# Kernel tuning notes

Hardware: AMD Instinct MI355X
Metric: run time of the kernel (lower is better)

Reference implementation:

```python
import jax, jax.numpy as jnp
import numpy as np

N_NODES = 50000
N_EDGES = 800000
IN, HID, OUT = 96, 96, 64


def setup_inputs() -> dict:
    key = jax.random.key(0)
    ks = jax.random.split(key, 12)
    x = jax.random.normal(ks[0], (N_NODES, IN), dtype=jnp.float32)
    src = jax.random.randint(ks[1], (N_EDGES,), 0, N_NODES, dtype=jnp.int32)
    dst = jax.random.randint(ks[2], (N_EDGES,), 0, N_NODES, dtype=jnp.int32)
    dims = [(IN, HID), (HID, HID), (HID, OUT)]
    params = {}
    for i, (din, dout) in enumerate(dims):
        s = 1.0 / np.sqrt(din)
        params[f"w_self{i}"] = jax.random.uniform(ks[3 + 3 * i], (dout, din), jnp.float32, -s, s)
        params[f"w_neigh{i}"] = jax.random.uniform(ks[4 + 3 * i], (dout, din), jnp.float32, -s, s)
        params[f"b{i}"] = jnp.zeros((dout,), jnp.float32)
    return {"x": x, "src": src, "dst": dst, **params}


def _sage_layer(h, src, dst, w_self, w_neigh, b):
    # mean aggregation of source-node features onto destination nodes
    msum = jax.ops.segment_sum(h[src], dst, num_segments=N_NODES)  # [N, d]
    deg = jax.ops.segment_sum(jnp.ones((src.shape[0],), h.dtype), dst, num_segments=N_NODES)
    hmean = msum / jnp.maximum(deg, 1.0)[:, None]
    return h @ w_self.T + hmean @ w_neigh.T + b


def reference(x, src, dst,
              w_self0, w_neigh0, b0,
              w_self1, w_neigh1, b1,
              w_self2, w_neigh2, b2):
    # Layer 0 + ReLU (dropout is identity in eval mode)
    h = jax.nn.relu(_sage_layer(x, src, dst, w_self0, w_neigh0, b0))
    # Layer 1 + ReLU
    h = jax.nn.relu(_sage_layer(h, src, dst, w_self1, w_neigh1, b1))
    # Final layer, no activation
    h = _sage_layer(h, src, dst, w_self2, w_neigh2, b2)
    return h
```

## Files before the change

kernel.cpp:

```cpp
#include <hip/hip_runtime.h>
#include <hip/hip_fp16.h>


#define DIN 96

typedef __attribute__((ext_vector_type(8))) short bf16x8;
typedef __attribute__((ext_vector_type(16))) float f32x16;

__global__ void zero_deg_kernel(int* __restrict__ p, int n) {
    int i = blockIdx.x * blockDim.x + threadIdx.x;
    if (i < n) p[i] = 0;
}

__global__ void deg_kernel(const int* __restrict__ dst, int* __restrict__ deg,
                           int* __restrict__ rank, int nE) {
    int i = blockIdx.x * blockDim.x + threadIdx.x;
    if (i < nE) rank[i] = atomicAdd(&deg[dst[i]], 1);
}

__global__ void block_sum_kernel(const int* __restrict__ deg, int* __restrict__ bsum, int nN) {
    __shared__ int s[256];
    const int tid = threadIdx.x;
    int i = blockIdx.x * 256 + tid;
    s[tid] = (i < nN) ? deg[i] : 0;
    __syncthreads();
    for (int d = 128; d > 0; d >>= 1) {
        if (tid < d) s[tid] += s[tid + d];
        __syncthreads();
    }
    if (tid == 0) bsum[blockIdx.x] = s[0];
}

__global__ void bsum_scan_kernel(int* __restrict__ bsum, int nB) {
    __shared__ int s[256];
    const int tid = threadIdx.x;
    int v = (tid < nB) ? bsum[tid] : 0;
    s[tid] = v;
    __syncthreads();
    for (int d = 1; d < 256; d <<= 1) {
        int t = (tid >= d) ? s[tid - d] : 0;
        __syncthreads();
        s[tid] += t;
        __syncthreads();
    }
    if (tid < nB) bsum[tid] = s[tid] - v;
}

__global__ void scan_apply_kernel(const int* __restrict__ deg, const int* __restrict__ bsum,
                                  int* __restrict__ offs, int nN) {
    __shared__ int s[256];
    const int tid = threadIdx.x;
    int i = blockIdx.x * 256 + tid;
    int v = (i < nN) ? deg[i] : 0;
    s[tid] = v;
    __syncthreads();
    for (int d = 1; d < 256; d <<= 1) {
        int t = (tid >= d) ? s[tid - d] : 0;
        __syncthreads();
        s[tid] += t;
        __syncthreads();
    }
    if (i < nN) offs[i] = bsum[blockIdx.x] + s[tid] - v;
}

__global__ void bucket_kernel(const int* __restrict__ src, const int* __restrict__ dst,
                              const int* __restrict__ offs, const int* __restrict__ rank,
                              unsigned short* __restrict__ esrc, int nE) {
    int e = blockIdx.x * blockDim.x + threadIdx.x;
    if (e < nE) esrc[offs[dst[e]] + rank[e]] = (unsigned short)src[e];
}

__global__ void tof16_kernel(const float* __restrict__ x, __half* __restrict__ xf, int n8) {
    int i = blockIdx.x * blockDim.x + threadIdx.x;
    if (i >= n8) return;
    float4 f0 = *reinterpret_cast<const float4*>(x + (size_t)i * 8);
    float4 f1 = *reinterpret_cast<const float4*>(x + (size_t)i * 8 + 4);
    union { __half2 h2[4]; float4 raw; } o;
    o.h2[0] = __float22half2_rn(make_float2(f0.x, f0.y));
    o.h2[1] = __float22half2_rn(make_float2(f0.z, f0.w));
    o.h2[2] = __float22half2_rn(make_float2(f1.x, f1.y));
    o.h2[3] = __float22half2_rn(make_float2(f1.z, f1.w));
    *reinterpret_cast<float4*>(xf + (size_t)i * 8) = o.raw;
}

__global__ void gather_kernel(const __half* __restrict__ hf, const unsigned short* __restrict__ esrc,
                              const int* __restrict__ offs, const int* __restrict__ deg,
                              __half* __restrict__ hmean, int nN) {
    int idx = blockIdx.x * blockDim.x + threadIdx.x;
    if (idx >= nN * 12) return;
    int n = idx / 12;
    int q = idx - n * 12;
    const int beg = offs[n];
    const int dg = deg[n];
    const int end = beg + dg;
    const __half* hq = hf + q * 8;

    union H8 { float4 raw; __half2 h2[4]; };
    float a0[8], a1[8], a2[8], a3[8];
#pragma unroll
    for (int k = 0; k < 8; ++k) { a0[k] = 0.f; a1[k] = 0.f; a2[k] = 0.f; a3[k] = 0.f; }

    int j = beg;
    for (; j + 4 <= end; j += 4) {
        int s0 = esrc[j], s1 = esrc[j + 1], s2 = esrc[j + 2], s3 = esrc[j + 3];
        H8 v0, v1, v2, v3;
        v0.raw = *reinterpret_cast<const float4*>(hq + (size_t)s0 * DIN);
        v1.raw = *reinterpret_cast<const float4*>(hq + (size_t)s1 * DIN);
        v2.raw = *reinterpret_cast<const float4*>(hq + (size_t)s2 * DIN);
        v3.raw = *reinterpret_cast<const float4*>(hq + (size_t)s3 * DIN);
#pragma unroll
        for (int k = 0; k < 4; ++k) {
            float2 f0 = __half22float2(v0.h2[k]);
            float2 f1 = __half22float2(v1.h2[k]);
            float2 f2 = __half22float2(v2.h2[k]);
            float2 f3 = __half22float2(v3.h2[k]);
            a0[2 * k] += f0.x; a0[2 * k + 1] += f0.y;
            a1[2 * k] += f1.x; a1[2 * k + 1] += f1.y;
            a2[2 * k] += f2.x; a2[2 * k + 1] += f2.y;
            a3[2 * k] += f3.x; a3[2 * k + 1] += f3.y;
        }
    }
    for (; j < end; ++j) {
        int s0 = esrc[j];
        H8 v0;
        v0.raw = *reinterpret_cast<const float4*>(hq + (size_t)s0 * DIN);
#pragma unroll
        for (int k = 0; k < 4; ++k) {
            float2 f0 = __half22float2(v0.h2[k]);
            a0[2 * k] += f0.x; a0[2 * k + 1] += f0.y;
        }
    }
    const float r = 1.0f / (float)max(dg, 1);
    union H8 o;
    o.h2[0] = __float22half2_rn(make_float2((a0[0]+a1[0]+a2[0]+a3[0])*r, (a0[1]+a1[1]+a2[1]+a3[1])*r));
    o.h2[1] = __float22half2_rn(make_float2((a0[2]+a1[2]+a2[2]+a3[2])*r, (a0[3]+a1[3]+a2[3]+a3[3])*r));
    o.h2[2] = __float22half2_rn(make_float2((a0[4]+a1[4]+a2[4]+a3[4])*r, (a0[5]+a1[5]+a2[5]+a3[5])*r));
    o.h2[3] = __float22half2_rn(make_float2((a0[6]+a1[6]+a2[6]+a3[6])*r, (a0[7]+a1[7]+a2[7]+a3[7])*r));
    *reinterpret_cast<float4*>(hmean + (size_t)n * DIN + q * 8) = o.raw;
}

__device__ __forceinline__ void fv8_to_hilo(const float* fv, bf16x8& hi, bf16x8& lo) {
    union { unsigned int u[4]; bf16x8 v; } H, L;
#pragma unroll
    for (int i = 0; i < 4; ++i) {
        unsigned u0 = __float_as_uint(fv[2 * i]);
        unsigned u1 = __float_as_uint(fv[2 * i + 1]);
        unsigned h0 = u0 & 0xFFFF0000u;
        unsigned h1 = u1 & 0xFFFF0000u;
        H.u[i] = h1 | (h0 >> 16);
        float l0 = fv[2 * i]     - __uint_as_float(h0);
        float l1 = fv[2 * i + 1] - __uint_as_float(h1);
        L.u[i] = (__float_as_uint(l1) & 0xFFFF0000u) | (__float_as_uint(l0) >> 16);
    }
    hi = H.v; lo = L.v;
}

template<int DOUT, int NP, bool RELU, bool WF16>
__global__ __launch_bounds__(256)
void sage_gemm_mfma(const float* __restrict__ hin, const __half* __restrict__ hm16,
                    const float* __restrict__ wself, const float* __restrict__ wneigh,
                    const float* __restrict__ bias, float* __restrict__ hout,
                    __half* __restrict__ fout, int nN) {
    __shared__ unsigned int WhiS[DOUT][100];
    __shared__ unsigned int WloS[DOUT][100];

    const int tid = threadIdx.x;
    const int n0 = blockIdx.x * 256;

    for (int c = tid; c < DOUT * 24; c += 256) {
        int r = c / 24, k8 = c - (c / 24) * 24;
        const float* srcw = (k8 < 12) ? (wself + (size_t)r * 96 + k8 * 8)
                                      : (wneigh + (size_t)r * 96 + (k8 - 12) * 8);
        float4 f0 = *reinterpret_cast<const float4*>(srcw);
        float4 f1 = *reinterpret_cast<const float4*>(srcw + 4);
        float fv[8] = {f0.x, f0.y, f0.z, f0.w, f1.x, f1.y, f1.z, f1.w};
        bf16x8 hi, lo;
        fv8_to_hilo(fv, hi, lo);
        *reinterpret_cast<bf16x8*>(&WhiS[r][k8 * 4]) = hi;
        *reinterpret_cast<bf16x8*>(&WloS[r][k8 * 4]) = lo;
    }
    __syncthreads();

    const int lane = tid & 63;
    const int w = tid >> 6;
    const int col = lane & 31;
    const int q = lane >> 5;
    const int mbase = n0 + w * 64;

    const int nA0 = min(mbase + col, nN - 1);
    const int nA1 = min(mbase + 32 + col, nN - 1);

    f32x16 acc[NP][2];
#pragma unroll
    for (int p = 0; p < NP; ++p) {
        f32x16 z = {};
        acc[p][0] = z;
        acc[p][1] = z;
    }

#pragma unroll
    for (int ks = 0; ks < 12; ++ks) {
        float fv0[8], fv1[8];
        if (ks < 6) {
            const float* s0 = hin + (size_t)nA0 * 96 + ks * 16 + q * 8;
            const float* s1 = hin + (size_t)nA1 * 96 + ks * 16 + q * 8;
            float4 a = *reinterpret_cast<const float4*>(s0);
            float4 b = *reinterpret_cast<const float4*>(s0 + 4);
            float4 c = *reinterpret_cast<const float4*>(s1);
            float4 d = *reinterpret_cast<const float4*>(s1 + 4);
            fv0[0]=a.x; fv0[1]=a.y; fv0[2]=a.z; fv0[3]=a.w;
            fv0[4]=b.x; fv0[5]=b.y; fv0[6]=b.z; fv0[7]=b.w;
            fv1[0]=c.x; fv1[1]=c.y; fv1[2]=c.z; fv1[3]=c.w;
            fv1[4]=d.x; fv1[5]=d.y; fv1[6]=d.z; fv1[7]=d.w;
        } else {
            const __half* s0 = hm16 + (size_t)nA0 * 96 + (ks - 6) * 16 + q * 8;
            const __half* s1 = hm16 + (size_t)nA1 * 96 + (ks - 6) * 16 + q * 8;
            union { float4 raw; __half2 h2[4]; } u0, u1;
            u0.raw = *reinterpret_cast<const float4*>(s0);
            u1.raw = *reinterpret_cast<const float4*>(s1);
#pragma unroll
            for (int k = 0; k < 4; ++k) {
                float2 f0 = __half22float2(u0.h2[k]);
                float2 f1 = __half22float2(u1.h2[k]);
                fv0[2 * k] = f0.x; fv0[2 * k + 1] = f0.y;
                fv1[2 * k] = f1.x; fv1[2 * k + 1] = f1.y;
            }
        }
        bf16x8 ahi0, alo0, ahi1, alo1;
        fv8_to_hilo(fv0, ahi0, alo0);
        fv8_to_hilo(fv1, ahi1, alo1);

#pragma unroll
        for (int p = 0; p < NP; ++p) {
            const bf16x8 whi = *reinterpret_cast<const bf16x8*>(&WhiS[p * 32 + col][ks * 8 + q * 4]);
            const bf16x8 wlo = *reinterpret_cast<const bf16x8*>(&WloS[p * 32 + col][ks * 8 + q * 4]);
            acc[p][0] = __builtin_amdgcn_mfma_f32_32x32x16_bf16(ahi0, whi, acc[p][0], 0, 0, 0);
            acc[p][0] = __builtin_amdgcn_mfma_f32_32x32x16_bf16(ahi0, wlo, acc[p][0], 0, 0, 0);
            acc[p][0] = __builtin_amdgcn_mfma_f32_32x32x16_bf16(alo0, whi, acc[p][0], 0, 0, 0);
            acc[p][1] = __builtin_amdgcn_mfma_f32_32x32x16_bf16(ahi1, whi, acc[p][1], 0, 0, 0);
            acc[p][1] = __builtin_amdgcn_mfma_f32_32x32x16_bf16(ahi1, wlo, acc[p][1], 0, 0, 0);
            acc[p][1] = __builtin_amdgcn_mfma_f32_32x32x16_bf16(alo1, whi, acc[p][1], 0, 0, 0);
        }
    }

#pragma unroll
    for (int p = 0; p < NP; ++p) {
        const int oc = p * 32 + col;
        const float bv = bias[oc];
#pragma unroll
        for (int i = 0; i < 16; ++i) {
            const int row = (i & 3) + 8 * (i >> 2) + 4 * q;
            int n = mbase + row;
            if (n < nN) {
                float v = acc[p][0][i] + bv;
                if (RELU) v = fmaxf(v, 0.f);
                hout[(size_t)n * DOUT + oc] = v;
                if (WF16) fout[(size_t)n * DOUT + oc] = __float2half_rn(v);
            }
            n = mbase + 32 + row;
            if (n < nN) {
                float v = acc[p][1][i] + bv;
                if (RELU) v = fmaxf(v, 0.f);
                hout[(size_t)n * DOUT + oc] = v;
                if (WF16) fout[(size_t)n * DOUT + oc] = __float2half_rn(v);
            }
        }
    }
}

extern "C" void kernel_launch(void* const* d_in, const int* in_sizes, int n_in,
                              void* d_out, int out_size, void* d_ws, size_t ws_size,
                              hipStream_t stream) {
    const float* x   = (const float*)d_in[0];
    const int*   src = (const int*)d_in[1];
    const int*   dst = (const int*)d_in[2];
    const float* ws0 = (const float*)d_in[3];
    const float* wn0 = (const float*)d_in[4];
    const float* b0  = (const float*)d_in[5];
    const float* ws1 = (const float*)d_in[6];
    const float* wn1 = (const float*)d_in[7];
    const float* b1  = (const float*)d_in[8];
    const float* ws2 = (const float*)d_in[9];
    const float* wn2 = (const float*)d_in[10];
    const float* b2  = (const float*)d_in[11];
    float* out = (float*)d_out;

    const int nN = in_sizes[0] / DIN;
    const int nE = in_sizes[1];
    const int nB = (nN + 255) / 256;

    int* deg  = (int*)d_ws;
    int* offs = deg + 50048;
    int* bsum = offs + 50048;
    int* rank = bsum + 256;
    unsigned short* esrc = (unsigned short*)(rank + nE);
    __half* hm16 = (__half*)(esrc + nE);
    float* hA    = (float*)(hm16 + (size_t)nN * DIN);
    float* hB    = hA + (size_t)nN * DIN;

    __half* f16buf = (__half*)d_out;

    zero_deg_kernel<<<nB, 256, 0, stream>>>(deg, nN);
    deg_kernel<<<(nE + 255) / 256, 256, 0, stream>>>(dst, deg, rank, nE);
    block_sum_kernel<<<nB, 256, 0, stream>>>(deg, bsum, nN);
    bsum_scan_kernel<<<1, 256, 0, stream>>>(bsum, nB);
    scan_apply_kernel<<<nB, 256, 0, stream>>>(deg, bsum, offs, nN);
    bucket_kernel<<<(nE + 255) / 256, 256, 0, stream>>>(src, dst, offs, rank, esrc, nE);

    const int ggrid = (nN * 12 + 255) / 256;
    const int mgrid = (nN + 255) / 256;

    tof16_kernel<<<ggrid, 256, 0, stream>>>(x, f16buf, nN * 12);
    gather_kernel<<<ggrid, 256, 0, stream>>>(f16buf, esrc, offs, deg, hm16, nN);
    sage_gemm_mfma<96, 3, true, true><<<mgrid, 256, 0, stream>>>(x, hm16, ws0, wn0, b0, hA, f16buf, nN);

    gather_kernel<<<ggrid, 256, 0, stream>>>(f16buf, esrc, offs, deg, hm16, nN);
    sage_gemm_mfma<96, 3, true, true><<<mgrid, 256, 0, stream>>>(hA, hm16, ws1, wn1, b1, hB, f16buf, nN);

    gather_kernel<<<ggrid, 256, 0, stream>>>(f16buf, esrc, offs, deg, hm16, nN);
    sage_gemm_mfma<64, 2, false, false><<<mgrid, 256, 0, stream>>>(hB, hm16, ws2, wn2, b2, out, nullptr, nN);
}
```

Before: 222.8 us.

## Use wave-per-node edge-parallel gather and fp16-only hidden activations in GEMMs

The gather kernel now assigns one 64-lane wave per node: 60 lanes cover 5 edges times 12 feature chunks at a time, and a cross-lane shuffle reduction sums the partial results. This is meant to balance uneven degrees and give more loads in flight per node. The GEMM now reads self features as fp16 and writes only the fp16 hidden output in place, dropping the fp32 hidden buffers and their reads and writes. The trade-off is lower precision on the self-feature path, including the input x, plus 4 idle lanes per wave and shuffle overhead.

```diff
diff --git a/kernel.cpp b/kernel.cpp
--- a/kernel.cpp
+++ b/kernel.cpp
@@ -83,60 +83,51 @@
     *reinterpret_cast<float4*>(xf + (size_t)i * 8) = o.raw;
 }
 
-__global__ void gather_kernel(const __half* __restrict__ hf, const unsigned short* __restrict__ esrc,
-                              const int* __restrict__ offs, const int* __restrict__ deg,
-                              __half* __restrict__ hmean, int nN) {
-    int idx = blockIdx.x * blockDim.x + threadIdx.x;
-    if (idx >= nN * 12) return;
-    int n = idx / 12;
-    int q = idx - n * 12;
+__global__ __launch_bounds__(256)
+void gather_kernel(const __half* __restrict__ hf, const unsigned short* __restrict__ esrc,
+                   const int* __restrict__ offs, const int* __restrict__ deg,
+                   __half* __restrict__ hmean, int nN) {
+    const int n = blockIdx.x * 4 + (threadIdx.x >> 6);
+    if (n >= nN) return;
+    const int lane = threadIdx.x & 63;
+    const int e = lane / 12;
+    const int q = lane - e * 12;
+    const bool active = lane < 60;
     const int beg = offs[n];
     const int dg = deg[n];
-    const int end = beg + dg;
-    const __half* hq = hf + q * 8;
-
-    union H8 { float4 raw; __half2 h2[4]; };
-    float a0[8], a1[8], a2[8], a3[8];
-#pragma unroll
-    for (int k = 0; k < 8; ++k) { a0[k] = 0.f; a1[k] = 0.f; a2[k] = 0.f; a3[k] = 0.f; }
-
-    int j = beg;
-    for (; j + 4 <= end; j += 4) {
-        int s0 = esrc[j], s1 = esrc[j + 1], s2 = esrc[j + 2], s3 = esrc[j + 3];
-        H8 v0, v1, v2, v3;
-        v0.raw = *reinterpret_cast<const float4*>(hq + (size_t)s0 * DIN);
-        v1.raw = *reinterpret_cast<const float4*>(hq + (size_t)s1 * DIN);
-        v2.raw = *reinterpret_cast<const float4*>(hq + (size_t)s2 * DIN);
-        v3.raw = *reinterpret_cast<const float4*>(hq + (size_t)s3 * DIN);
-#pragma unroll
-        for (int k = 0; k < 4; ++k) {
-            float2 f0 = __half22float2(v0.h2[k]);
-            float2 f1 = __half22float2(v1.h2[k]);
-            float2 f2 = __half22float2(v2.h2[k]);
-            float2 f3 = __half22float2(v3.h2[k]);
-            a0[2 * k] += f0.x; a0[2 * k + 1] += f0.y;
-            a1[2 * k] += f1.x; a1[2 * k + 1] += f1.y;
-            a2[2 * k] += f2.x; a2[2 * k + 1] += f2.y;
-            a3[2 * k] += f3.x; a3[2 * k + 1] += f3.y;
+
+    float acc[8] = {0.f, 0.f, 0.f, 0.f, 0.f, 0.f, 0.f, 0.f};
+    for (int it = 0; it < dg; it += 5) {
+        const int j = it + e;
+        if (active && j < dg) {
+            const int s = esrc[beg + j];
+            union { float4 raw; __half2 h2[4]; } v;
+            v.raw = *reinterpret_cast<const float4*>(hf + (size_t)s * DIN + q * 8);
+#pragma unroll
+            for (int k = 0; k < 4; ++k) {
+                float2 f = __half22float2(v.h2[k]);
+                acc[2 * k] += f.x;
+                acc[2 * k + 1] += f.y;
+            }
         }
     }
-    for (; j < end; ++j) {
-        int s0 = esrc[j];
-        H8 v0;
-        v0.raw = *reinterpret_cast<const float4*>(hq + (size_t)s0 * DIN);
-#pragma unroll
-        for (int k = 0; k < 4; ++k) {
-            float2 f0 = __half22float2(v0.h2[k]);
-            a0[2 * k] += f0.x; a0[2 * k + 1] += f0.y;
-        }
-    }
-    const float r = 1.0f / (float)max(dg, 1);
-    union H8 o;
-    o.h2[0] = __float22half2_rn(make_float2((a0[0]+a1[0]+a2[0]+a3[0])*r, (a0[1]+a1[1]+a2[1]+a3[1])*r));
-    o.h2[1] = __float22half2_rn(make_float2((a0[2]+a1[2]+a2[2]+a3[2])*r, (a0[3]+a1[3]+a2[3]+a3[3])*r));
-    o.h2[2] = __float22half2_rn(make_float2((a0[4]+a1[4]+a2[4]+a3[4])*r, (a0[5]+a1[5]+a2[5]+a3[5])*r));
-    o.h2[3] = __float22half2_rn(make_float2((a0[6]+a1[6]+a2[6]+a3[6])*r, (a0[7]+a1[7]+a2[7]+a3[7])*r));
-    *reinterpret_cast<float4*>(hmean + (size_t)n * DIN + q * 8) = o.raw;
+    float tot[8];
+#pragma unroll
+    for (int k = 0; k < 8; ++k) {
+        float a = acc[k];
+        float s1 = a + __shfl(a, lane + 12);
+        float s2 = s1 + __shfl(s1, lane + 24);
+        tot[k] = s2 + __shfl(a, lane + 48);
+    }
+    if (lane < 12) {
+        const float r = 1.0f / (float)max(dg, 1);
+        union { __half2 h2[4]; float4 raw; } o;
+        o.h2[0] = __float22half2_rn(make_float2(tot[0] * r, tot[1] * r));
+        o.h2[1] = __float22half2_rn(make_float2(tot[2] * r, tot[3] * r));
+        o.h2[2] = __float22half2_rn(make_float2(tot[4] * r, tot[5] * r));
+        o.h2[3] = __float22half2_rn(make_float2(tot[6] * r, tot[7] * r));
+        *reinterpret_cast<float4*>(hmean + (size_t)n * DIN + q * 8) = o.raw;
+    }
 }
 
 __device__ __forceinline__ void fv8_to_hilo(const float* fv, bf16x8& hi, bf16x8& lo) {
@@ -155,12 +146,12 @@
     hi = H.v; lo = L.v;
 }
 
-template<int DOUT, int NP, bool RELU, bool WF16>
+template<int DOUT, int NP, bool RELU, bool FINAL>
 __global__ __launch_bounds__(256)
-void sage_gemm_mfma(const float* __restrict__ hin, const __half* __restrict__ hm16,
+void sage_gemm_mfma(const __half* __restrict__ hp, const __half* __restrict__ hm,
                     const float* __restrict__ wself, const float* __restrict__ wneigh,
-                    const float* __restrict__ bias, float* __restrict__ hout,
-                    __half* __restrict__ fout, int nN) {
+                    const float* __restrict__ bias, float* __restrict__ fout,
+                    __half* __restrict__ hout, int nN) {
     __shared__ unsigned int WhiS[DOUT][100];
     __shared__ unsigned int WloS[DOUT][100];
 
@@ -200,31 +191,20 @@
 
 #pragma unroll
     for (int ks = 0; ks < 12; ++ks) {
+        const __half* s0 = (ks < 6) ? (hp + (size_t)nA0 * 96 + ks * 16 + q * 8)
+                                    : (hm + (size_t)nA0 * 96 + (ks - 6) * 16 + q * 8);
+        const __half* s1 = (ks < 6) ? (hp + (size_t)nA1 * 96 + ks * 16 + q * 8)
+                                    : (hm + (size_t)nA1 * 96 + (ks - 6) * 16 + q * 8);
+        union { float4 raw; __half2 h2[4]; } u0, u1;
+        u0.raw = *reinterpret_cast<const float4*>(s0);
+        u1.raw = *reinterpret_cast<const float4*>(s1);
         float fv0[8], fv1[8];
-        if (ks < 6) {
-            const float* s0 = hin + (size_t)nA0 * 96 + ks * 16 + q * 8;
-            const float* s1 = hin + (size_t)nA1 * 96 + ks * 16 + q * 8;
-            float4 a = *reinterpret_cast<const float4*>(s0);
-            float4 b = *reinterpret_cast<const float4*>(s0 + 4);
-            float4 c = *reinterpret_cast<const float4*>(s1);
-            float4 d = *reinterpret_cast<const float4*>(s1 + 4);
-            fv0[0]=a.x; fv0[1]=a.y; fv0[2]=a.z; fv0[3]=a.w;
-            fv0[4]=b.x; fv0[5]=b.y; fv0[6]=b.z; fv0[7]=b.w;
-            fv1[0]=c.x; fv1[1]=c.y; fv1[2]=c.z; fv1[3]=c.w;
-            fv1[4]=d.x; fv1[5]=d.y; fv1[6]=d.z; fv1[7]=d.w;
-        } else {
-            const __half* s0 = hm16 + (size_t)nA0 * 96 + (ks - 6) * 16 + q * 8;
-            const __half* s1 = hm16 + (size_t)nA1 * 96 + (ks - 6) * 16 + q * 8;
-            union { float4 raw; __half2 h2[4]; } u0, u1;
-            u0.raw = *reinterpret_cast<const float4*>(s0);
-            u1.raw = *reinterpret_cast<const float4*>(s1);
-#pragma unroll
-            for (int k = 0; k < 4; ++k) {
-                float2 f0 = __half22float2(u0.h2[k]);
-                float2 f1 = __half22float2(u1.h2[k]);
-                fv0[2 * k] = f0.x; fv0[2 * k + 1] = f0.y;
-                fv1[2 * k] = f1.x; fv1[2 * k + 1] = f1.y;
-            }
+#pragma unroll
+        for (int k = 0; k < 4; ++k) {
+            float2 f0 = __half22float2(u0.h2[k]);
+            float2 f1 = __half22float2(u1.h2[k]);
+            fv0[2 * k] = f0.x; fv0[2 * k + 1] = f0.y;
+            fv1[2 * k] = f1.x; fv1[2 * k + 1] = f1.y;
         }
         bf16x8 ahi0, alo0, ahi1, alo1;
         fv8_to_hilo(fv0, ahi0, alo0);
@@ -254,15 +234,15 @@
             if (n < nN) {
                 float v = acc[p][0][i] + bv;
                 if (RELU) v = fmaxf(v, 0.f);
-                hout[(size_t)n * DOUT + oc] = v;
-                if (WF16) fout[(size_t)n * DOUT + oc] = __float2half_rn(v);
+                if (FINAL) fout[(size_t)n * DOUT + oc] = v;
+                else       hout[(size_t)n * DOUT + oc] = __float2half_rn(v);
             }
             n = mbase + 32 + row;
             if (n < nN) {
                 float v = acc[p][1][i] + bv;
                 if (RELU) v = fmaxf(v, 0.f);
-                hout[(size_t)n * DOUT + oc] = v;
-                if (WF16) fout[(size_t)n * DOUT + oc] = __float2half_rn(v);
+                if (FINAL) fout[(size_t)n * DOUT + oc] = v;
+                else       hout[(size_t)n * DOUT + oc] = __float2half_rn(v);
             }
         }
     }
@@ -294,11 +274,8 @@
     int* bsum = offs + 50048;
     int* rank = bsum + 256;
     unsigned short* esrc = (unsigned short*)(rank + nE);
-    __half* hm16 = (__half*)(esrc + nE);
-    float* hA    = (float*)(hm16 + (size_t)nN * DIN);
-    float* hB    = hA + (size_t)nN * DIN;
-
-    __half* f16buf = (__half*)d_out;
+    __half* hp16 = (__half*)(esrc + nE);
+    __half* hm16 = hp16 + (size_t)nN * DIN;
 
     zero_deg_kernel<<<nB, 256, 0, stream>>>(deg, nN);
     deg_kernel<<<(nE + 255) / 256, 256, 0, stream>>>(dst, deg, rank, nE);
@@ -307,16 +284,17 @@
     scan_apply_kernel<<<nB, 256, 0, stream>>>(deg, bsum, offs, nN);
     bucket_kernel<<<(nE + 255) / 256, 256, 0, stream>>>(src, dst, offs, rank, esrc, nE);
 
-    const int ggrid = (nN * 12 + 255) / 256;
+    const int cgrid = (nN * 12 + 255) / 256;
+    const int wgrid = (nN + 3) / 4;
     const int mgrid = (nN + 255) / 256;
 
-    tof16_kernel<<<ggrid, 256, 0, stream>>>(x, f16buf, nN * 12);
-    gather_kernel<<<ggrid, 256, 0, stream>>>(f16buf, esrc, offs, deg, hm16, nN);
-    sage_gemm_mfma<96, 3, true, true><<<mgrid, 256, 0, stream>>>(x, hm16, ws0, wn0, b0, hA, f16buf, nN);
-
-    gather_kernel<<<ggrid, 256, 0, stream>>>(f16buf, esrc, offs, deg, hm16, nN);
-    sage_gemm_mfma<96, 3, true, true><<<mgrid, 256, 0, stream>>>(hA, hm16, ws1, wn1, b1, hB, f16buf, nN);
-
-    gather_kernel<<<ggrid, 256, 0, stream>>>(f16buf, esrc, offs, deg, hm16, nN);
-    sage_gemm_mfma<64, 2, false, false><<<mgrid, 256, 0, stream>>>(hB, hm16, ws2, wn2, b2, out, nullptr, nN);
-}
+    tof16_kernel<<<cgrid, 256, 0, stream>>>(x, hp16, nN * 12);
+    gather_kernel<<<wgrid, 256, 0, stream>>>(hp16, esrc, offs, deg, hm16, nN);
+    sage_gemm_mfma<96, 3, true, false><<<mgrid, 256, 0, stream>>>(hp16, hm16, ws0, wn0, b0, nullptr, hp16, nN);
+
+    gather_kernel<<<wgrid, 256, 0, stream>>>(hp16, esrc, offs, deg, hm16, nN);
+    sage_gemm_mfma<96, 3, true, false><<<mgrid, 256, 0, stream>>>(hp16, hm16, ws1, wn1, b1, nullptr, hp16, nN);
+
+    gather_kernel<<<wgrid, 256, 0, stream>>>(hp16, esrc, offs, deg, hm16, nN);
+    sage_gemm_mfma<64, 2, false, true><<<mgrid, 256, 0, stream>>>(hp16, hm16, ws2, wn2, b2, out, nullptr, nN);
+}
```

New measurement: 236.4 us. 6.1% more time.
